# Optimization experiments

Hardware: AMD Instinct MI355X
Metric: run time of the kernel (lower is better)

Reference implementation:

```python
import jax, jax.numpy as jnp
import numpy as np

N = 1048576
H = 5  # hidden_dim

def setup_inputs() -> dict:
    key = jax.random.key(0)
    ks = jax.random.split(key, 7)
    # Kaiming normal (fan_in, relu gain sqrt(2)) per-layer, biases zero, stacked over N models
    W1 = jax.random.normal(ks[0], (N, H), dtype=jnp.float32) * np.sqrt(2.0 / 1.0)
    b1 = jnp.zeros((N, H), dtype=jnp.float32)
    W2 = jax.random.normal(ks[1], (N, H, H), dtype=jnp.float32) * np.sqrt(2.0 / H)
    b2 = jnp.zeros((N, H), dtype=jnp.float32)
    W3 = jax.random.normal(ks[2], (N, H), dtype=jnp.float32) * np.sqrt(2.0 / H)
    b3 = jnp.zeros((N, 1), dtype=jnp.float32)
    x = jax.random.normal(ks[3], (N,), dtype=jnp.float32)
    return {"x": x, "W1": W1, "b1": b1, "W2": W2, "b2": b2, "W3": W3, "b3": b3}

def reference(x, W1, b1, W2, b2, W3, b3):
    # model i: scalar x[i] -> Linear(1,H) -> ELU -> Linear(H,H) -> ELU -> Linear(H,1)
    h1 = jax.nn.elu(x[:, None] * W1 + b1)                      # (N, H)
    h2 = jax.nn.elu(jnp.einsum('nh,noh->no', h1, W2) + b2)     # (N, H)  W2[n] is (out,in)
    out = jnp.sum(h2 * W3, axis=-1, keepdims=True) + b3        # (N, 1)
    return out
```

## Files before the change

### kernel.cpp

```cpp
#include <hip/hip_runtime.h>
#include <math.h>


#define H 5
#define MPB 256

__global__ __launch_bounds__(256, 6) void perturbnet_kernel(
    const float* __restrict__ x,
    const float* __restrict__ W1,
    const float* __restrict__ b1,
    const float* __restrict__ W2,
    const float* __restrict__ b2,
    const float* __restrict__ W3,
    const float* __restrict__ b3,
    float* __restrict__ out,
    int N)
{
    __shared__ __align__(16) float sW2[MPB * H * H];

    const int tid = threadIdx.x;
    const int blockBase = blockIdx.x * MPB;
    const int gid = blockBase + tid;

    if (blockBase + MPB <= N) {
        const float xv = x[gid];

        float w1[H], bb1[H], bb2[H], w3[H];
        #pragma unroll
        for (int h = 0; h < H; ++h) w1[h]  = W1[(size_t)gid * H + h];
        #pragma unroll
        for (int h = 0; h < H; ++h) bb1[h] = b1[(size_t)gid * H + h];
        #pragma unroll
        for (int h = 0; h < H; ++h) bb2[h] = b2[(size_t)gid * H + h];
        #pragma unroll
        for (int h = 0; h < H; ++h) w3[h]  = W3[(size_t)gid * H + h];
        const float bb3 = b3[gid];

        {
            const float4* s = reinterpret_cast<const float4*>(W2 + (size_t)blockBase * H * H);
            float4* d = reinterpret_cast<float4*>(sW2);
            #pragma unroll
            for (int i = tid; i < (MPB * H * H) / 4; i += MPB) d[i] = s[i];
        }
        __syncthreads();

        float h1[H];
        #pragma unroll
        for (int h = 0; h < H; ++h) {
            float v = fmaf(xv, w1[h], bb1[h]);
            h1[h] = v > 0.0f ? v : (__expf(v) - 1.0f);
        }

        float h2[H];
        #pragma unroll
        for (int o = 0; o < H; ++o) {
            float acc = bb2[o];
            #pragma unroll
            for (int h = 0; h < H; ++h)
                acc = fmaf(h1[h], sW2[tid * (H * H) + o * H + h], acc);
            h2[o] = acc > 0.0f ? acc : (__expf(acc) - 1.0f);
        }

        float acc = bb3;
        #pragma unroll
        for (int o = 0; o < H; ++o)
            acc = fmaf(h2[o], w3[o], acc);

        out[gid] = acc;
    } else {
        if (gid < N) {
            const float xv = x[gid];
            float h1[H];
            #pragma unroll
            for (int h = 0; h < H; ++h) {
                float v = fmaf(xv, W1[(size_t)gid * H + h], b1[(size_t)gid * H + h]);
                h1[h] = v > 0.0f ? v : (__expf(v) - 1.0f);
            }
            float h2[H];
            #pragma unroll
            for (int o = 0; o < H; ++o) {
                float acc = b2[(size_t)gid * H + o];
                #pragma unroll
                for (int h = 0; h < H; ++h)
                    acc = fmaf(h1[h], W2[(size_t)gid * H * H + o * H + h], acc);
                h2[o] = acc > 0.0f ? acc : (__expf(acc) - 1.0f);
            }
            float acc = b3[gid];
            #pragma unroll
            for (int o = 0; o < H; ++o)
                acc = fmaf(h2[o], W3[(size_t)gid * H + o], acc);
            out[gid] = acc;
        }
    }
}

extern "C" void kernel_launch(void* const* d_in, const int* in_sizes, int n_in,
                              void* d_out, int out_size, void* d_ws, size_t ws_size,
                              hipStream_t stream) {
    const float* x  = (const float*)d_in[0];
    const float* W1 = (const float*)d_in[1];
    const float* b1 = (const float*)d_in[2];
    const float* W2 = (const float*)d_in[3];
    const float* b2 = (const float*)d_in[4];
    const float* W3 = (const float*)d_in[5];
    const float* b3 = (const float*)d_in[6];
    float* out = (float*)d_out;

    const int N = in_sizes[0];
    const int grid = (N + MPB - 1) / MPB;
    perturbnet_kernel<<<grid, MPB, 0, stream>>>(x, W1, b1, W2, b2, W3, b3, out, N);
}
```

Measured before the change: 225.4 us.

## Process four models per thread with float4 vector loads, drop shared staging

Each thread now computes four consecutive models and reads all parameters through float4 loads from contiguous per-thread spans. The shared-memory staging of W2 and the block barrier are removed, and W2 is streamed in register groups. This targets the many scalar strided loads and the barrier overhead. In exchange, registers per thread rise and there are fewer threads, with large per-lane strides in each load instruction.

```diff
diff --git a/kernel.cpp b/kernel.cpp
--- a/kernel.cpp
+++ b/kernel.cpp
@@ -3,9 +3,11 @@
 
 
 #define H 5
-#define MPB 256
+#define TPB 256
+#define MPT 4
+#define MPB (TPB * MPT)
 
-__global__ __launch_bounds__(256, 6) void perturbnet_kernel(
+__global__ __launch_bounds__(TPB, 4) void perturbnet_kernel(
     const float* __restrict__ x,
     const float* __restrict__ W1,
     const float* __restrict__ b1,
@@ -16,80 +18,115 @@
     float* __restrict__ out,
     int N)
 {
-    __shared__ __align__(16) float sW2[MPB * H * H];
+    const int t   = blockIdx.x * TPB + threadIdx.x;
+    const int m0  = t * MPT;
 
-    const int tid = threadIdx.x;
-    const int blockBase = blockIdx.x * MPB;
-    const int gid = blockBase + tid;
+    if (m0 + MPT <= N && (N % MPT) == 0) {
+        const float4 xv = reinterpret_cast<const float4*>(x)[t];
 
-    if (blockBase + MPB <= N) {
-        const float xv = x[gid];
+        float w1[MPT * H], bb1[MPT * H];
+        {
+            const float4* p = reinterpret_cast<const float4*>(W1 + (size_t)m0 * H);
+            const float4* q = reinterpret_cast<const float4*>(b1 + (size_t)m0 * H);
+            #pragma unroll
+            for (int j = 0; j < 5; ++j) {
+                float4 a = p[j];
+                w1[4*j+0]=a.x; w1[4*j+1]=a.y; w1[4*j+2]=a.z; w1[4*j+3]=a.w;
+            }
+            #pragma unroll
+            for (int j = 0; j < 5; ++j) {
+                float4 a = q[j];
+                bb1[4*j+0]=a.x; bb1[4*j+1]=a.y; bb1[4*j+2]=a.z; bb1[4*j+3]=a.w;
+            }
+        }
 
-        float w1[H], bb1[H], bb2[H], w3[H];
+        float h1[MPT * H];
+        const float xs[MPT] = {xv.x, xv.y, xv.z, xv.w};
         #pragma unroll
-        for (int h = 0; h < H; ++h) w1[h]  = W1[(size_t)gid * H + h];
-        #pragma unroll
-        for (int h = 0; h < H; ++h) bb1[h] = b1[(size_t)gid * H + h];
-        #pragma unroll
-        for (int h = 0; h < H; ++h) bb2[h] = b2[(size_t)gid * H + h];
-        #pragma unroll
-        for (int h = 0; h < H; ++h) w3[h]  = W3[(size_t)gid * H + h];
-        const float bb3 = b3[gid];
+        for (int m = 0; m < MPT; ++m)
+            #pragma unroll
+            for (int h = 0; h < H; ++h) {
+                float v = fmaf(xs[m], w1[m*H+h], bb1[m*H+h]);
+                h1[m*H+h] = v > 0.0f ? v : (__expf(v) - 1.0f);
+            }
+
+        float acc[MPT * H];
+        {
+            const float4* q = reinterpret_cast<const float4*>(b2 + (size_t)m0 * H);
+            #pragma unroll
+            for (int j = 0; j < 5; ++j) {
+                float4 a = q[j];
+                acc[4*j+0]=a.x; acc[4*j+1]=a.y; acc[4*j+2]=a.z; acc[4*j+3]=a.w;
+            }
+        }
 
         {
-            const float4* s = reinterpret_cast<const float4*>(W2 + (size_t)blockBase * H * H);
-            float4* d = reinterpret_cast<float4*>(sW2);
+            const float4* p = reinterpret_cast<const float4*>(W2 + (size_t)m0 * H * H);
             #pragma unroll
-            for (int i = tid; i < (MPB * H * H) / 4; i += MPB) d[i] = s[i];
-        }
-        __syncthreads();
-
-        float h1[H];
-        #pragma unroll
-        for (int h = 0; h < H; ++h) {
-            float v = fmaf(xv, w1[h], bb1[h]);
-            h1[h] = v > 0.0f ? v : (__expf(v) - 1.0f);
+            for (int grp = 0; grp < 5; ++grp) {
+                float w2g[20];
+                #pragma unroll
+                for (int j = 0; j < 5; ++j) {
+                    float4 a = p[grp*5 + j];
+                    w2g[4*j+0]=a.x; w2g[4*j+1]=a.y; w2g[4*j+2]=a.z; w2g[4*j+3]=a.w;
+                }
+                #pragma unroll
+                for (int k = 0; k < 20; ++k) {
+                    const int g = grp*20 + k;
+                    const int m = g / (H*H);
+                    const int r = g % (H*H);
+                    const int o = r / H;
+                    const int i = r % H;
+                    acc[m*H+o] = fmaf(w2g[k], h1[m*H+i], acc[m*H+o]);
+                }
+            }
         }
 
-        float h2[H];
+        float w3[MPT * H];
+        {
+            const float4* p = reinterpret_cast<const float4*>(W3 + (size_t)m0 * H);
+            #pragma unroll
+            for (int j = 0; j < 5; ++j) {
+                float4 a = p[j];
+                w3[4*j+0]=a.x; w3[4*j+1]=a.y; w3[4*j+2]=a.z; w3[4*j+3]=a.w;
+            }
+        }
+        const float4 b3v = reinterpret_cast<const float4*>(b3)[t];
+        const float b3s[MPT] = {b3v.x, b3v.y, b3v.z, b3v.w};
+
+        float res[MPT];
         #pragma unroll
-        for (int o = 0; o < H; ++o) {
-            float acc = bb2[o];
-            #pragma unroll
-            for (int h = 0; h < H; ++h)
-                acc = fmaf(h1[h], sW2[tid * (H * H) + o * H + h], acc);
-            h2[o] = acc > 0.0f ? acc : (__expf(acc) - 1.0f);
-        }
-
-        float acc = bb3;
-        #pragma unroll
-        for (int o = 0; o < H; ++o)
-            acc = fmaf(h2[o], w3[o], acc);
-
-        out[gid] = acc;
-    } else {
-        if (gid < N) {
-            const float xv = x[gid];
-            float h1[H];
-            #pragma unroll
-            for (int h = 0; h < H; ++h) {
-                float v = fmaf(xv, W1[(size_t)gid * H + h], b1[(size_t)gid * H + h]);
-                h1[h] = v > 0.0f ? v : (__expf(v) - 1.0f);
-            }
-            float h2[H];
+        for (int m = 0; m < MPT; ++m) {
+            float s = b3s[m];
             #pragma unroll
             for (int o = 0; o < H; ++o) {
-                float acc = b2[(size_t)gid * H + o];
-                #pragma unroll
+                float v = acc[m*H+o];
+                v = v > 0.0f ? v : (__expf(v) - 1.0f);
+                s = fmaf(v, w3[m*H+o], s);
+            }
+            res[m] = s;
+        }
+        float4 ov; ov.x=res[0]; ov.y=res[1]; ov.z=res[2]; ov.w=res[3];
+        reinterpret_cast<float4*>(out)[t] = ov;
+    } else {
+        #pragma unroll
+        for (int m = m0; m < m0 + MPT; ++m) {
+            if (m >= N) break;
+            const float xv1 = x[m];
+            float h1s[H];
+            for (int h = 0; h < H; ++h) {
+                float v = fmaf(xv1, W1[(size_t)m*H+h], b1[(size_t)m*H+h]);
+                h1s[h] = v > 0.0f ? v : (__expf(v) - 1.0f);
+            }
+            float r = b3[m];
+            for (int o = 0; o < H; ++o) {
+                float a = b2[(size_t)m*H+o];
                 for (int h = 0; h < H; ++h)
-                    acc = fmaf(h1[h], W2[(size_t)gid * H * H + o * H + h], acc);
-                h2[o] = acc > 0.0f ? acc : (__expf(acc) - 1.0f);
+                    a = fmaf(h1s[h], W2[(size_t)m*H*H + o*H + h], a);
+                a = a > 0.0f ? a : (__expf(a) - 1.0f);
+                r = fmaf(a, W3[(size_t)m*H+o], r);
             }
-            float acc = b3[gid];
-            #pragma unroll
-            for (int o = 0; o < H; ++o)
-                acc = fmaf(h2[o], W3[(size_t)gid * H + o], acc);
-            out[gid] = acc;
+            out[m] = r;
         }
     }
 }
@@ -108,5 +145,5 @@
 
     const int N = in_sizes[0];
     const int grid = (N + MPB - 1) / MPB;
-    perturbnet_kernel<<<grid, MPB, 0, stream>>>(x, W1, b1, W2, b2, W3, b3, out, N);
+    perturbnet_kernel<<<grid, TPB, 0, stream>>>(x, W1, b1, W2, b2, W3, b3, out, N);
 }
```

New measurement: 246.3 us. +9.3%, slower.
